# Optimization experiments

Hardware: AMD Instinct MI355X
Metric: run time of the kernel (lower is better)

Reference implementation:

```python
import jax, jax.numpy as jnp
import numpy as np

N, H, W = 4, 64, 64
OUT_CH, NUM_PAST, LAYERS = 128, 4, 8


def _layer_dims():
    # (c_in, c_out, kernel, pad) for each of the 8 deformable convs
    dims = [(NUM_PAST * OUT_CH, 256, 1, 0), (256, 128, 3, 1)]
    for _ in range(LAYERS - 3):
        dims.append((128, 128, 3, 1))
    dims.append((128, OUT_CH, 3, 1))
    return dims


def setup_inputs() -> dict:
    key = jax.random.key(0)
    keys = jax.random.split(key, 64)
    inp = {"x": jax.random.normal(keys[0], (N, NUM_PAST * OUT_CH, H, W), jnp.float32)}
    dims = _layer_dims()
    for i, (cin, cout, k, p) in enumerate(dims):
        inp[f"off{i}"] = jax.random.normal(keys[1 + i], (N, 2 * k * k, H, W), jnp.float32)
    for i, (cin, cout, k, p) in enumerate(dims):
        fan_in = cin * k * k
        inp[f"w{i}"] = jax.random.normal(keys[20 + i], (cout, cin, k, k), jnp.float32) * np.sqrt(2.0 / fan_in)
        inp[f"b{i}"] = jnp.zeros((cout,), jnp.float32)
    return inp


def _bilinear(img, py, px):
    # img: [N,C,H,W]; py/px: [N,H,W] float sampling coords. Zero padding outside.
    _, _, Hh, Ww = img.shape
    y0 = jnp.floor(py)
    x0 = jnp.floor(px)
    y1, x1 = y0 + 1.0, x0 + 1.0
    wy1 = py - y0
    wy0 = 1.0 - wy1
    wx1 = px - x0
    wx0 = 1.0 - wx1

    def corner(yc, xc, wgt):
        valid = (yc >= 0) & (yc < Hh) & (xc >= 0) & (xc < Ww)
        yi = jnp.clip(yc, 0, Hh - 1).astype(jnp.int32)
        xi = jnp.clip(xc, 0, Ww - 1).astype(jnp.int32)
        vals = jax.vmap(lambda im, yy, xx: im[:, yy, xx])(img, yi, xi)  # [N,C,H,W]
        return vals * (wgt * valid)[:, None]

    return (corner(y0, x0, wy0 * wx0) + corner(y0, x1, wy0 * wx1)
            + corner(y1, x0, wy1 * wx0) + corner(y1, x1, wy1 * wx1))


def deform_conv2d(x, offset, weight, bias, pad):
    # torchvision DeformConv2d (1 group, 1 offset group), stride 1, dilation 1.
    n, c, h, w = x.shape
    cout, _, K, _ = weight.shape
    off = offset.reshape(n, K * K, 2, h, w)  # per tap: [dy, dx]
    base_y = jnp.arange(h, dtype=x.dtype)[:, None]
    base_x = jnp.arange(w, dtype=x.dtype)[None, :]
    out = jnp.broadcast_to(bias[None, :, None, None], (n, cout, h, w)).astype(x.dtype)
    for k in range(K * K):  # fixed small kernel loop (1 or 9 taps)
        kh, kw = divmod(k, K)
        py = base_y + (kh - pad) + off[:, k, 0]
        px = base_x + (kw - pad) + off[:, k, 1]
        s = _bilinear(x, py, px)  # [N,C,H,W]
        out = out + jnp.einsum('nchw,oc->nohw', s, weight[:, :, kh, kw])
    return out


def reference(x, off0, off1, off2, off3, off4, off5, off6, off7,
              w0, b0, w1, b1, w2, b2, w3, b3, w4, b4, w5, b5, w6, b6, w7, b7):
    offs = [off0, off1, off2, off3, off4, off5, off6, off7]
    ws = [w0, w1, w2, w3, w4, w5, w6, w7]
    bs = [b0, b1, b2, b3, b4, b5, b6, b7]
    for i, (cin, cout, k, p) in enumerate(_layer_dims()):
        x = jax.nn.relu(deform_conv2d(x, offs[i], ws[i], bs[i], p))
    return x
```

## Files before the change

kernel.cpp:

```cpp
#include <hip/hip_runtime.h>

typedef _Float16 f16x8 __attribute__((ext_vector_type(8)));
typedef _Float16 f16x4 __attribute__((ext_vector_type(4)));
typedef float f32x4 __attribute__((ext_vector_type(4)));


__global__ __launch_bounds__(256) void nchw2nhwc(const float* __restrict__ in,
                                                 float* __restrict__ out, int C) {
    const int ctiles = C >> 5;
    const int ct = blockIdx.x % ctiles;
    const int xt = blockIdx.x / ctiles;
    const int y = blockIdx.y, n = blockIdx.z;
    const int c0 = ct * 32, x0 = xt * 32;
    __shared__ float tile[32][33];
    const int tx = threadIdx.x & 31, tr = threadIdx.x >> 5;
#pragma unroll
    for (int r = 0; r < 32; r += 8) {
        const int c = c0 + tr + r;
        tile[tr + r][tx] = in[(((n * C + c) << 6) + y) * 64 + x0 + tx];
    }
    __syncthreads();
#pragma unroll
    for (int r = 0; r < 32; r += 8) {
        const int x = x0 + tr + r;
        out[((((n << 6) + y) * 64) + x) * C + c0 + tx] = tile[tx][tr + r];
    }
}

__global__ __launch_bounds__(256) void nhwc2nchw(const float* __restrict__ in,
                                                 float* __restrict__ out, int C) {
    const int ctiles = C >> 5;
    const int ct = blockIdx.x % ctiles;
    const int xt = blockIdx.x / ctiles;
    const int y = blockIdx.y, n = blockIdx.z;
    const int c0 = ct * 32, x0 = xt * 32;
    __shared__ float tile[32][33];
    const int tx = threadIdx.x & 31, tr = threadIdx.x >> 5;
#pragma unroll
    for (int r = 0; r < 32; r += 8) {
        const int x = x0 + tr + r;
        tile[tr + r][tx] = in[((((n << 6) + y) * 64) + x) * C + c0 + tx];
    }
    __syncthreads();
#pragma unroll
    for (int r = 0; r < 32; r += 8) {
        const int c = c0 + tr + r;
        out[(((n * C + c) << 6) + y) * 64 + x0 + tx] = tile[tx][tr + r];
    }
}

__global__ __launch_bounds__(256) void prep_wfrag(const float* __restrict__ w,
                                                  _Float16* __restrict__ wtf,
                                                  int CIN, int COUT, int KK, int total) {
    const int idx = blockIdx.x * 256 + threadIdx.x;
    if (idx >= total) return;
    const int lane = idx & 63;
    int r = idx >> 6;
    const int NCO16 = COUT >> 4;
    const int g = r % NCO16;
    r /= NCO16;
    const int NC = CIN >> 5;
    const int co = g * 16 + (lane & 15);
    const int ci0 = (r % NC) * 32 + (lane >> 4) * 8;
    const int k = r / NC;
    f16x8 hv, lv;
#pragma unroll
    for (int j = 0; j < 8; ++j) {
        const float v = w[(co * CIN + ci0 + j) * KK + k];
        const _Float16 h = (_Float16)v;
        hv[j] = h;
        lv[j] = (_Float16)(v - (float)h);
    }
    const size_t base = ((size_t)(r * NCO16 + g)) * 1024 + lane * 8;
    *(f16x8*)&wtf[base] = hv;
    *(f16x8*)&wtf[base + 512] = lv;
}

struct PixSt {
    float w0, w1, w2, w3;
    const float *p00, *p01, *p10, *p11;
};

struct ASet {
    float4 A0[4];
    float cw[4];
};

template <int TAPS, int CIN, int COUTF>
__global__ __launch_bounds__(512) void dconv_mfma(const float* __restrict__ in,
                                                  const float* __restrict__ off,
                                                  const _Float16* __restrict__ wtf,
                                                  const float* __restrict__ bias,
                                                  float* __restrict__ out) {
    constexpr int KS = (TAPS == 9) ? 3 : 1;
    constexpr int PAD = (TAPS == 9) ? 1 : 0;
    constexpr int NC = CIN / 32;
    constexpr int NCO16 = COUTF / 16;
    constexpr int TOTAL_IT = TAPS * NC;

    __shared__ __align__(16) _Float16 sAh[2][64 * 40];
    __shared__ __align__(16) _Float16 sAl[2][64 * 40];

    const int t = threadIdx.x;
    const int bx0 = blockIdx.x;
    const int bx = (bx0 & 7) * 32 + (bx0 >> 3);
    const int coy = blockIdx.y;
    const int n = bx >> 6, y = bx & 63;

    const int ppx = t >> 3;
    const int j4 = (t & 7) * 4;

    const int lane = t & 63, wv = t >> 6;
    const int l15 = lane & 15, lq = lane >> 4;
    const int gbase = (coy * 128 + wv * 16) >> 4;

    PixSt q0;

    auto mkcoef = [&](PixSt& q, int k, float dy, float dx) {
        const int kh = k / KS, kw = k - kh * KS;
        const float py = (float)(y + kh - PAD) + dy;
        const float pxc = (float)(ppx + kw - PAD) + dx;
        const float y0f = floorf(py), x0f = floorf(pxc);
        const int iy0 = (int)y0f, ix0 = (int)x0f;
        const int iy1 = iy0 + 1, ix1 = ix0 + 1;
        const float wy1 = py - y0f, wy0 = 1.f - wy1;
        const float wx1 = pxc - x0f, wx0 = 1.f - wx1;
        const bool vy0 = (iy0 >= 0) & (iy0 < 64), vy1 = (iy1 >= 0) & (iy1 < 64);
        const bool vx0 = (ix0 >= 0) & (ix0 < 64), vx1 = (ix1 >= 0) & (ix1 < 64);
        q.w0 = (vy0 & vx0) ? wy0 * wx0 : 0.f;
        q.w1 = (vy0 & vx1) ? wy0 * wx1 : 0.f;
        q.w2 = (vy1 & vx0) ? wy1 * wx0 : 0.f;
        q.w3 = (vy1 & vx1) ? wy1 * wx1 : 0.f;
        const int cy0 = min(max(iy0, 0), 63), cy1 = min(max(iy1, 0), 63);
        const int cx0 = min(max(ix0, 0), 63), cx1 = min(max(ix1, 0), 63);
        q.p00 = in + (size_t)(((n << 6) + cy0) * 64 + cx0) * CIN + j4;
        q.p01 = in + (size_t)(((n << 6) + cy0) * 64 + cx1) * CIN + j4;
        q.p10 = in + (size_t)(((n << 6) + cy1) * 64 + cx0) * CIN + j4;
        q.p11 = in + (size_t)(((n << 6) + cy1) * 64 + cx1) * CIN + j4;
    };

    auto oidx = [&](int k) {
        return ((n * 2 * TAPS + 2 * k) * 64 + y) * 64 + ppx;
    };

    ASet S0, S1;
    f16x8 bh0, bl0, bh1, bl1;

    auto loadA = [&](ASet& S, int c) {
        const int o = c * 32;
        S.A0[0] = *(const float4*)(q0.p00 + o);
        S.A0[1] = *(const float4*)(q0.p01 + o);
        S.A0[2] = *(const float4*)(q0.p10 + o);
        S.A0[3] = *(const float4*)(q0.p11 + o);
        S.cw[0] = q0.w0; S.cw[1] = q0.w1; S.cw[2] = q0.w2; S.cw[3] = q0.w3;
    };

    auto loadB = [&](f16x8& bh, f16x8& bl, int k, int c) {
        const size_t rw = ((size_t)((k * NC + c) * NCO16) + gbase) * 1024 + lane * 8;
        bh = *(const f16x8*)&wtf[rw];
        bl = *(const f16x8*)&wtf[rw + 512];
    };

    auto write_chunk = [&](const ASet& S, int buf) {
        float v0[4];
        v0[0] = S.cw[0] * S.A0[0].x + S.cw[1] * S.A0[1].x + S.cw[2] * S.A0[2].x + S.cw[3] * S.A0[3].x;
        v0[1] = S.cw[0] * S.A0[0].y + S.cw[1] * S.A0[1].y + S.cw[2] * S.A0[2].y + S.cw[3] * S.A0[3].y;
        v0[2] = S.cw[0] * S.A0[0].z + S.cw[1] * S.A0[1].z + S.cw[2] * S.A0[2].z + S.cw[3] * S.A0[3].z;
        v0[3] = S.cw[0] * S.A0[0].w + S.cw[1] * S.A0[1].w + S.cw[2] * S.A0[2].w + S.cw[3] * S.A0[3].w;
        f16x4 hv0, lv0;
#pragma unroll
        for (int j = 0; j < 4; ++j) {
            const _Float16 h0 = (_Float16)v0[j];
            hv0[j] = h0;
            lv0[j] = (_Float16)(v0[j] - (float)h0);
        }
        *(f16x4*)&sAh[buf][ppx * 40 + j4] = hv0;
        *(f16x4*)&sAl[buf][ppx * 40 + j4] = lv0;
    };

    mkcoef(q0, 0, off[oidx(0)], off[oidx(0) + 4096]);
    float dyn0 = 0.f, dxn0 = 0.f;
    if (TAPS > 1) { dyn0 = off[oidx(1)]; dxn0 = off[oidx(1) + 4096]; }
    loadA(S0, 0); loadB(bh0, bl0, 0, 0);
    loadA(S1, 1); loadB(bh1, bl1, 0, 1);
    int kq = 0, cq = 1;

    f32x4 acc[4] = {};

    auto body = [&](ASet& S, f16x8& bh, f16x8& bl, int buf, int it) {
        write_chunk(S, buf);
        const bool more = (it + 2 < TOTAL_IT);
        if (more) {
            int c2 = cq + 1, k2 = kq;
            if (c2 == NC) {
                c2 = 0; k2 = kq + 1;
                mkcoef(q0, k2, dyn0, dxn0);
                if (k2 + 1 < TAPS) {
                    dyn0 = off[oidx(k2 + 1)];
                    dxn0 = off[oidx(k2 + 1) + 4096];
                }
            }
            loadA(S, c2);
            kq = k2; cq = c2;
        }
        asm volatile("s_waitcnt lgkmcnt(0)\n\ts_barrier" ::: "memory");

        f16x8 ah[4], al[4];
#pragma unroll
        for (int mi = 0; mi < 4; ++mi) {
            const int ar = mi * 16 + l15;
            ah[mi] = *(const f16x8*)&sAh[buf][ar * 40 + lq * 8];
            al[mi] = *(const f16x8*)&sAl[buf][ar * 40 + lq * 8];
        }
#pragma unroll
        for (int mi = 0; mi < 4; ++mi) {
            acc[mi] = __builtin_amdgcn_mfma_f32_16x16x32_f16(ah[mi], bh, acc[mi], 0, 0, 0);
            acc[mi] = __builtin_amdgcn_mfma_f32_16x16x32_f16(ah[mi], bl, acc[mi], 0, 0, 0);
            acc[mi] = __builtin_amdgcn_mfma_f32_16x16x32_f16(al[mi], bh, acc[mi], 0, 0, 0);
        }
        if (more) loadB(bh, bl, kq, cq);
    };

    for (int it = 0; it < TOTAL_IT; it += 2) {
        body(S0, bh0, bl0, 0, it);
        body(S1, bh1, bl1, 1, it + 1);
    }

    const size_t pixbase = (size_t)bx * 64;
    {
        const int co = coy * 128 + wv * 16 + l15;
        const float bv = bias[co];
#pragma unroll
        for (int mi = 0; mi < 4; ++mi) {
#pragma unroll
            for (int r = 0; r < 4; ++r) {
                const int pxl = mi * 16 + lq * 4 + r;
                out[(pixbase + pxl) * COUTF + co] = fmaxf(acc[mi][r] + bv, 0.f);
            }
        }
    }
}

extern "C" void kernel_launch(void* const* d_in, const int* in_sizes, int n_in,
                              void* d_out, int out_size, void* d_ws, size_t ws_size,
                              hipStream_t stream) {
    (void)in_sizes; (void)n_in; (void)out_size; (void)ws_size;
    const float* x = (const float*)d_in[0];
    const float* offs[8];
    const float* wsrc[8];
    const float* bs[8];
    for (int i = 0; i < 8; ++i) {
        offs[i] = (const float*)d_in[1 + i];
        wsrc[i] = (const float*)d_in[9 + 2 * i];
        bs[i] = (const float*)d_in[10 + 2 * i];
    }
    float* bufA = (float*)d_ws;
    float* bufB = (float*)((char*)d_ws + 33554432u);
    _Float16* wt = (_Float16*)((char*)d_ws + 50331648u);
    const size_t wo[8] = {0, 262144, 851968, 1146880, 1441792, 1736704, 2031616, 2326528};
    const int cins[8] = {512, 256, 128, 128, 128, 128, 128, 128};
    const int couts[8] = {256, 128, 128, 128, 128, 128, 128, 128};
    const int kks[8] = {1, 9, 9, 9, 9, 9, 9, 9};

    nchw2nhwc<<<dim3((512 / 32) * 2, 64, 4), 256, 0, stream>>>(x, bufA, 512);
    for (int i = 0; i < 8; ++i) {
        const int total = kks[i] * (cins[i] / 32) * (couts[i] / 16) * 64;
        prep_wfrag<<<(total + 255) / 256, 256, 0, stream>>>(wsrc[i], wt + wo[i],
                                                            cins[i], couts[i], kks[i], total);
    }
    dconv_mfma<1, 512, 256><<<dim3(256, 2), 512, 0, stream>>>(bufA, offs[0], wt + wo[0], bs[0], bufB);
    dconv_mfma<9, 256, 128><<<dim3(256, 1), 512, 0, stream>>>(bufB, offs[1], wt + wo[1], bs[1], bufA);
    dconv_mfma<9, 128, 128><<<dim3(256, 1), 512, 0, stream>>>(bufA, offs[2], wt + wo[2], bs[2], bufB);
    dconv_mfma<9, 128, 128><<<dim3(256, 1), 512, 0, stream>>>(bufB, offs[3], wt + wo[3], bs[3], bufA);
    dconv_mfma<9, 128, 128><<<dim3(256, 1), 512, 0, stream>>>(bufA, offs[4], wt + wo[4], bs[4], bufB);
    dconv_mfma<9, 128, 128><<<dim3(256, 1), 512, 0, stream>>>(bufB, offs[5], wt + wo[5], bs[5], bufA);
    dconv_mfma<9, 128, 128><<<dim3(256, 1), 512, 0, stream>>>(bufA, offs[6], wt + wo[6], bs[6], bufB);
    dconv_mfma<9, 128, 128><<<dim3(256, 1), 512, 0, stream>>>(bufB, offs[7], wt + wo[7], bs[7], bufA);
    nhwc2nchw<<<dim3((128 / 32) * 2, 64, 4), 256, 0, stream>>>(bufA, (float*)d_out, 128);
}
```

Before: 290.1 us.

## Double block size to 1024 threads, splitting pixel rows across wave halves

Raises the deformable conv block from 512 to 1024 threads. Each thread now gathers 2 channels instead of 4, and each wave computes 2 pixel M-tiles instead of 4, with the upper 8 waves handling the second 32 pixels. The aim is more waves in flight to hide the latency of the bilinear gathers, plus fewer registers per thread. In exchange the gathers become narrower float2 loads, B-fragment loads are duplicated across the two wave halves, and a barrier over 16 waves costs more.

```diff
diff --git a/kernel.cpp b/kernel.cpp
--- a/kernel.cpp
+++ b/kernel.cpp
@@ -2,6 +2,7 @@
 
 typedef _Float16 f16x8 __attribute__((ext_vector_type(8)));
 typedef _Float16 f16x4 __attribute__((ext_vector_type(4)));
+typedef _Float16 f16x2 __attribute__((ext_vector_type(2)));
 typedef float f32x4 __attribute__((ext_vector_type(4)));
 
 
@@ -82,16 +83,16 @@
 };
 
 struct ASet {
-    float4 A0[4];
+    float2 A0[4];
     float cw[4];
 };
 
 template <int TAPS, int CIN, int COUTF>
-__global__ __launch_bounds__(512) void dconv_mfma(const float* __restrict__ in,
-                                                  const float* __restrict__ off,
-                                                  const _Float16* __restrict__ wtf,
-                                                  const float* __restrict__ bias,
-                                                  float* __restrict__ out) {
+__global__ __launch_bounds__(1024) void dconv_mfma(const float* __restrict__ in,
+                                                   const float* __restrict__ off,
+                                                   const _Float16* __restrict__ wtf,
+                                                   const float* __restrict__ bias,
+                                                   float* __restrict__ out) {
     constexpr int KS = (TAPS == 9) ? 3 : 1;
     constexpr int PAD = (TAPS == 9) ? 1 : 0;
     constexpr int NC = CIN / 32;
@@ -107,12 +108,13 @@
     const int coy = blockIdx.y;
     const int n = bx >> 6, y = bx & 63;
 
-    const int ppx = t >> 3;
-    const int j4 = (t & 7) * 4;
+    const int ppx = t >> 4;
+    const int j2 = (t & 15) * 2;
 
     const int lane = t & 63, wv = t >> 6;
     const int l15 = lane & 15, lq = lane >> 4;
-    const int gbase = (coy * 128 + wv * 16) >> 4;
+    const int pxh = (wv >> 3) * 32;
+    const int gbase = coy * 8 + (wv & 7);
 
     PixSt q0;
 
@@ -133,10 +135,10 @@
         q.w3 = (vy1 & vx1) ? wy1 * wx1 : 0.f;
         const int cy0 = min(max(iy0, 0), 63), cy1 = min(max(iy1, 0), 63);
         const int cx0 = min(max(ix0, 0), 63), cx1 = min(max(ix1, 0), 63);
-        q.p00 = in + (size_t)(((n << 6) + cy0) * 64 + cx0) * CIN + j4;
-        q.p01 = in + (size_t)(((n << 6) + cy0) * 64 + cx1) * CIN + j4;
-        q.p10 = in + (size_t)(((n << 6) + cy1) * 64 + cx0) * CIN + j4;
-        q.p11 = in + (size_t)(((n << 6) + cy1) * 64 + cx1) * CIN + j4;
+        q.p00 = in + (size_t)(((n << 6) + cy0) * 64 + cx0) * CIN + j2;
+        q.p01 = in + (size_t)(((n << 6) + cy0) * 64 + cx1) * CIN + j2;
+        q.p10 = in + (size_t)(((n << 6) + cy1) * 64 + cx0) * CIN + j2;
+        q.p11 = in + (size_t)(((n << 6) + cy1) * 64 + cx1) * CIN + j2;
     };
 
     auto oidx = [&](int k) {
@@ -148,10 +150,10 @@
 
     auto loadA = [&](ASet& S, int c) {
         const int o = c * 32;
-        S.A0[0] = *(const float4*)(q0.p00 + o);
-        S.A0[1] = *(const float4*)(q0.p01 + o);
-        S.A0[2] = *(const float4*)(q0.p10 + o);
-        S.A0[3] = *(const float4*)(q0.p11 + o);
+        S.A0[0] = *(const float2*)(q0.p00 + o);
+        S.A0[1] = *(const float2*)(q0.p01 + o);
+        S.A0[2] = *(const float2*)(q0.p10 + o);
+        S.A0[3] = *(const float2*)(q0.p11 + o);
         S.cw[0] = q0.w0; S.cw[1] = q0.w1; S.cw[2] = q0.w2; S.cw[3] = q0.w3;
     };
 
@@ -162,20 +164,18 @@
     };
 
     auto write_chunk = [&](const ASet& S, int buf) {
-        float v0[4];
+        float v0[2];
         v0[0] = S.cw[0] * S.A0[0].x + S.cw[1] * S.A0[1].x + S.cw[2] * S.A0[2].x + S.cw[3] * S.A0[3].x;
         v0[1] = S.cw[0] * S.A0[0].y + S.cw[1] * S.A0[1].y + S.cw[2] * S.A0[2].y + S.cw[3] * S.A0[3].y;
-        v0[2] = S.cw[0] * S.A0[0].z + S.cw[1] * S.A0[1].z + S.cw[2] * S.A0[2].z + S.cw[3] * S.A0[3].z;
-        v0[3] = S.cw[0] * S.A0[0].w + S.cw[1] * S.A0[1].w + S.cw[2] * S.A0[2].w + S.cw[3] * S.A0[3].w;
-        f16x4 hv0, lv0;
-#pragma unroll
-        for (int j = 0; j < 4; ++j) {
+        f16x2 hv0, lv0;
+#pragma unroll
+        for (int j = 0; j < 2; ++j) {
             const _Float16 h0 = (_Float16)v0[j];
             hv0[j] = h0;
             lv0[j] = (_Float16)(v0[j] - (float)h0);
         }
-        *(f16x4*)&sAh[buf][ppx * 40 + j4] = hv0;
-        *(f16x4*)&sAl[buf][ppx * 40 + j4] = lv0;
+        *(f16x2*)&sAh[buf][ppx * 40 + j2] = hv0;
+        *(f16x2*)&sAl[buf][ppx * 40 + j2] = lv0;
     };
 
     mkcoef(q0, 0, off[oidx(0)], off[oidx(0) + 4096]);
@@ -185,7 +185,7 @@
     loadA(S1, 1); loadB(bh1, bl1, 0, 1);
     int kq = 0, cq = 1;
 
-    f32x4 acc[4] = {};
+    f32x4 acc[2] = {};
 
     auto body = [&](ASet& S, f16x8& bh, f16x8& bl, int buf, int it) {
         write_chunk(S, buf);
@@ -205,15 +205,15 @@
         }
         asm volatile("s_waitcnt lgkmcnt(0)\n\ts_barrier" ::: "memory");
 
-        f16x8 ah[4], al[4];
-#pragma unroll
-        for (int mi = 0; mi < 4; ++mi) {
-            const int ar = mi * 16 + l15;
+        f16x8 ah[2], al[2];
+#pragma unroll
+        for (int mi = 0; mi < 2; ++mi) {
+            const int ar = pxh + mi * 16 + l15;
             ah[mi] = *(const f16x8*)&sAh[buf][ar * 40 + lq * 8];
             al[mi] = *(const f16x8*)&sAl[buf][ar * 40 + lq * 8];
         }
 #pragma unroll
-        for (int mi = 0; mi < 4; ++mi) {
+        for (int mi = 0; mi < 2; ++mi) {
             acc[mi] = __builtin_amdgcn_mfma_f32_16x16x32_f16(ah[mi], bh, acc[mi], 0, 0, 0);
             acc[mi] = __builtin_amdgcn_mfma_f32_16x16x32_f16(ah[mi], bl, acc[mi], 0, 0, 0);
             acc[mi] = __builtin_amdgcn_mfma_f32_16x16x32_f16(al[mi], bh, acc[mi], 0, 0, 0);
@@ -228,13 +228,13 @@
 
     const size_t pixbase = (size_t)bx * 64;
     {
-        const int co = coy * 128 + wv * 16 + l15;
+        const int co = coy * 128 + (wv & 7) * 16 + l15;
         const float bv = bias[co];
 #pragma unroll
-        for (int mi = 0; mi < 4; ++mi) {
+        for (int mi = 0; mi < 2; ++mi) {
 #pragma unroll
             for (int r = 0; r < 4; ++r) {
-                const int pxl = mi * 16 + lq * 4 + r;
+                const int pxl = pxh + mi * 16 + lq * 4 + r;
                 out[(pixbase + pxl) * COUTF + co] = fmaxf(acc[mi][r] + bv, 0.f);
             }
         }
@@ -268,13 +268,13 @@
         prep_wfrag<<<(total + 255) / 256, 256, 0, stream>>>(wsrc[i], wt + wo[i],
                                                             cins[i], couts[i], kks[i], total);
     }
-    dconv_mfma<1, 512, 256><<<dim3(256, 2), 512, 0, stream>>>(bufA, offs[0], wt + wo[0], bs[0], bufB);
-    dconv_mfma<9, 256, 128><<<dim3(256, 1), 512, 0, stream>>>(bufB, offs[1], wt + wo[1], bs[1], bufA);
-    dconv_mfma<9, 128, 128><<<dim3(256, 1), 512, 0, stream>>>(bufA, offs[2], wt + wo[2], bs[2], bufB);
-    dconv_mfma<9, 128, 128><<<dim3(256, 1), 512, 0, stream>>>(bufB, offs[3], wt + wo[3], bs[3], bufA);
-    dconv_mfma<9, 128, 128><<<dim3(256, 1), 512, 0, stream>>>(bufA, offs[4], wt + wo[4], bs[4], bufB);
-    dconv_mfma<9, 128, 128><<<dim3(256, 1), 512, 0, stream>>>(bufB, offs[5], wt + wo[5], bs[5], bufA);
-    dconv_mfma<9, 128, 128><<<dim3(256, 1), 512, 0, stream>>>(bufA, offs[6], wt + wo[6], bs[6], bufB);
-    dconv_mfma<9, 128, 128><<<dim3(256, 1), 512, 0, stream>>>(bufB, offs[7], wt + wo[7], bs[7], bufA);
+    dconv_mfma<1, 512, 256><<<dim3(256, 2), 1024, 0, stream>>>(bufA, offs[0], wt + wo[0], bs[0], bufB);
+    dconv_mfma<9, 256, 128><<<dim3(256, 1), 1024, 0, stream>>>(bufB, offs[1], wt + wo[1], bs[1], bufA);
+    dconv_mfma<9, 128, 128><<<dim3(256, 1), 1024, 0, stream>>>(bufA, offs[2], wt + wo[2], bs[2], bufB);
+    dconv_mfma<9, 128, 128><<<dim3(256, 1), 1024, 0, stream>>>(bufB, offs[3], wt + wo[3], bs[3], bufA);
+    dconv_mfma<9, 128, 128><<<dim3(256, 1), 1024, 0, stream>>>(bufA, offs[4], wt + wo[4], bs[4], bufB);
+    dconv_mfma<9, 128, 128><<<dim3(256, 1), 1024, 0, stream>>>(bufB, offs[5], wt + wo[5], bs[5], bufA);
+    dconv_mfma<9, 128, 128><<<dim3(256, 1), 1024, 0, stream>>>(bufA, offs[6], wt + wo[6], bs[6], bufB);
+    dconv_mfma<9, 128, 128><<<dim3(256, 1), 1024, 0, stream>>>(bufB, offs[7], wt + wo[7], bs[7], bufA);
     nhwc2nchw<<<dim3((128 / 32) * 2, 64, 4), 256, 0, stream>>>(bufA, (float*)d_out, 128);
 }
```

After: 347.3 us. +19.7%, slower.
